# Performance work log

Measured on AMD Instinct MI355X. Metric: run time of the kernel, lower is better.

The kernel has to match this reference:

```python
import jax, jax.numpy as jnp
import numpy as np
from jax import lax

B, C, H, W = 256, 64, 48, 48   # batch, in_channels, spatial_dim, spatial_dim
E = 5                           # num_experts (ConditionalConv2D default)
DIM = 64 + 1                    # n_regulators + 1


def setup_inputs() -> dict:
    key = jax.random.key(0)
    ks = jax.random.split(key, 24)
    def n(k, shape, s=0.05):
        return jax.random.normal(k, shape, jnp.float32) * s
    inp = {
        "spatial_maps": jax.random.normal(ks[0], (B, C, H, W), jnp.float32),
        "cluster_info": jax.random.randint(ks[1], (B,), 0, C),
        # ConditionalConv2D (1x1, num_experts=5)
        "expert_w": n(ks[2], (E, C, C)),          # [experts, out_c, in_c] (1x1 squeezed)
        "cond_b": n(ks[3], (C,)),
        "route_emb": n(ks[4], (C, 4 * C)),        # Embedding(num_clusters=C, pool_emb=4C)
        "route_W": n(ks[5], (E, 8 * C)),          # Linear(2*pool_emb -> E)
        "route_b": n(ks[6], (E,)),
        # weight-normed conv stack (v, g, bias, prelu-a)
        "v1": n(ks[7], (32, C, 3, 3)),  "g1": jnp.ones((32,), jnp.float32),  "cb1": n(ks[8], (32,)),  "a1": jnp.array(0.1, jnp.float32),
        "v2": n(ks[9], (64, 32, 3, 3)), "g2": jnp.ones((64,), jnp.float32),  "cb2": n(ks[10], (64,)), "a2": jnp.array(0.1, jnp.float32),
        "v3": n(ks[11], (128, 64, 3, 3)), "g3": jnp.ones((128,), jnp.float32), "cb3": n(ks[12], (128,)), "a3": jnp.array(0.1, jnp.float32),
        # cluster embedding + alpha + MLP
        "emb2": n(ks[13], (C, 128)),
        "alpha": jnp.array(1.0, jnp.float32),
        "mW1": n(ks[14], (64, 128)), "mb1": n(ks[15], (64,)), "a4": jnp.array(0.1, jnp.float32),
        "mW2": n(ks[16], (32, 64)),  "mb2": n(ks[17], (32,)), "a5": jnp.array(0.1, jnp.float32),
        "mW3": n(ks[18], (DIM, 32)), "mb3": n(ks[19], (DIM,)),
    }
    return inp


def _wn(v, g):
    # weight_norm over all dims except 0 (torch default dim=0)
    nrm = jnp.sqrt((v * v).sum((1, 2, 3)))
    return v * (g / nrm)[:, None, None, None]


def _conv(x, w, b):
    y = lax.conv_general_dilated(x, w, (1, 1), 'SAME',
                                 dimension_numbers=('NCHW', 'OIHW', 'NCHW'))
    return y + b[None, :, None, None]


def _prelu(x, a):
    return jnp.where(x >= 0, x, a * x)


def _mpool(x):
    return lax.reduce_window(x, -jnp.inf, lax.max, (1, 1, 2, 2), (1, 1, 2, 2), 'VALID')


def reference(spatial_maps, cluster_info, expert_w, cond_b, route_emb, route_W, route_b,
              v1, g1, cb1, a1, v2, g2, cb2, a2, v3, g3, cb3, a3,
              emb2, alpha, mW1, mb1, a4, mW2, mb2, a5, mW3, mb3):
    x = spatial_maps
    # routing: adaptive avg pool (2,2), flatten, concat cluster embedding, linear, sigmoid
    pooled = x.reshape(B, C, 2, H // 2, 2, W // 2).mean((3, 5)).reshape(B, 4 * C)
    feat = jnp.concatenate([pooled, route_emb[cluster_info]], axis=1)      # [B, 8C]
    rw = jax.nn.sigmoid(feat @ route_W.T + route_b)                        # [B, E]
    # per-sample expert-mixed 1x1 kernel, applied as batched 1x1 conv
    kern = jnp.einsum('be,eoi->boi', rw, expert_w)                         # [B, C, C]
    cc = jnp.einsum('boi,bihw->bohw', kern, x) + cond_b[None, :, None, None]
    out = jax.nn.sigmoid(cc) * x                                           # attention gate
    # dense conv stack
    h = _mpool(_prelu(_conv(out, _wn(v1, g1), cb1), a1))
    h = _mpool(_prelu(_conv(h, _wn(v2, g2), cb2), a2))
    h = _mpool(_prelu(_conv(h, _wn(v3, g3), cb3), a3))
    h = h.mean((2, 3))                                                      # AdaptiveAvgPool2d(1)+Flatten -> [B,128]
    h = h + emb2[cluster_info] * alpha
    # MLP head
    h = _prelu(h @ mW1.T + mb1, a4)
    h = _prelu(h @ mW2.T + mb2, a5)
    return h @ mW3.T + mb3                                                  # [B, DIM]
```

## Files before the change

### kernel.cpp

```cpp
#include <hip/hip_runtime.h>


typedef _Float16 f16;
typedef f16 f16x8 __attribute__((ext_vector_type(8)));
typedef f16 f16x4 __attribute__((ext_vector_type(4)));
typedef f16 f16x2 __attribute__((ext_vector_type(2)));
typedef __fp16 h16x2 __attribute__((ext_vector_type(2)));
typedef float f32x4 __attribute__((ext_vector_type(4)));

constexpr size_t OFF_POOLED = 0;
constexpr size_t OFF_KERN   = 65536;
constexpr size_t OFF_W1     = 65536 + 1048576;
constexpr size_t OFF_W2     = OFF_W1 + 32*64*12;
constexpr size_t OFF_W3     = OFF_W2 + 64*32*12;
constexpr size_t OFF_H1     = OFF_W3 + 128*64*12;

__device__ __forceinline__ float sigmoidf_(float z) {
    return __builtin_amdgcn_rcpf(1.0f + __expf(-z));
}

__device__ __forceinline__ f16x2 pkrtz(float a, float b) {
    h16x2 r = __builtin_amdgcn_cvt_pkrtz(a, b);
    f16x2 o; o[0] = (f16)r[0]; o[1] = (f16)r[1];
    return o;
}

__device__ __forceinline__ void store_slot8(f16* glds, int row, int sc, int icg, const float* c) {
    f16x2 p0 = pkrtz(c[0], c[1]);
    f16x2 p1 = pkrtz(c[2], c[3]);
    f16x2 p2 = pkrtz(c[4], c[5]);
    f16x2 p3 = pkrtz(c[6], c[7]);
    f16x8 hv = { p0[0], p0[1], p1[0], p1[1], p2[0], p2[1], p3[0], p3[1] };
    *(f16x8*)&glds[(row * 50 + sc) * 64 + ((icg ^ (sc & 7)) << 3)] = hv;
}

__global__ void __launch_bounds__(64)
k_prep(const float* __restrict__ x,
       const float* __restrict__ v1, const float* __restrict__ g1,
       const float* __restrict__ v2, const float* __restrict__ g2,
       const float* __restrict__ v3, const float* __restrict__ g3,
       float* __restrict__ ws)
{
    const int blk = blockIdx.x;
    const int lane = threadIdx.x;
    if (blk < 16384) {
        const float4* p = (const float4*)(x + (size_t)blk * 2304);
        float a0 = 0.f, a1 = 0.f, a2 = 0.f, a3 = 0.f;
        #pragma unroll
        for (int j = 0; j < 9; j++) {
            int i = lane + 64 * j;
            int row = i / 12, cg = i - 12 * row;
            float4 v = p[i];
            float s = v.x + v.y + v.z + v.w;
            bool hq = (row >= 24), wq = (cg >= 6);
            a0 += (!hq && !wq) ? s : 0.f;
            a1 += (!hq &&  wq) ? s : 0.f;
            a2 += ( hq && !wq) ? s : 0.f;
            a3 += ( hq &&  wq) ? s : 0.f;
        }
        #pragma unroll
        for (int off = 32; off; off >>= 1) {
            a0 += __shfl_down(a0, off);
            a1 += __shfl_down(a1, off);
            a2 += __shfl_down(a2, off);
            a3 += __shfl_down(a3, off);
        }
        if (lane == 0) {
            int b = blk >> 6, c = blk & 63;
            float* d = ws + OFF_POOLED + (size_t)b * 256 + c * 4;
            d[0] = a0 * (1.0f / 576.0f);
            d[1] = a1 * (1.0f / 576.0f);
            d[2] = a2 * (1.0f / 576.0f);
            d[3] = a3 * (1.0f / 576.0f);
        }
    } else {
        int bo = blk - 16384;
        const float* v; const float* g; int IC, oc; int which;
        if (bo < 32)       { v = v1; g = g1; oc = bo;      IC = 64; which = 1; }
        else if (bo < 96)  { v = v2; g = g2; oc = bo - 32; IC = 32; which = 2; }
        else               { v = v3; g = g3; oc = bo - 96; IC = 64; which = 3; }
        int n = IC * 9;
        const float* vo = v + (size_t)oc * n;
        float s = 0.0f;
        for (int i = lane; i < n; i += 64) { float xv = vo[i]; s += xv * xv; }
        #pragma unroll
        for (int off = 32; off; off >>= 1) s += __shfl_down(s, off);
        float tot = __shfl(s, 0);
        float sc = g[oc] / sqrtf(tot);
        if (which == 1) {
            f16* o1 = (f16*)(ws + OFF_W1);
            for (int i = lane; i < n; i += 64) {
                int ic = i / 9, kk = i - ic * 9;
                o1[kk * 2048 + oc * 64 + (ic ^ ((oc & 7) << 3))] = (f16)(vo[i] * sc);
            }
        } else if (which == 2) {
            f16* o2 = (f16*)(ws + OFF_W2);
            for (int i = lane; i < n; i += 64) {
                int ic = i / 9, kk = i - ic * 9;
                o2[(kk * 64 + oc) * 32 + ic] = (f16)(vo[i] * sc);
            }
        } else {
            f16* o3 = (f16*)(ws + OFF_W3);
            for (int i = lane; i < n; i += 64) {
                int ic = i / 9, kk = i - ic * 9;
                o3[(kk * 128 + oc) * 64 + ic] = (f16)(vo[i] * sc);
            }
        }
    }
}

__global__ void k_route(const int* __restrict__ cluster,
                        const float* __restrict__ route_emb,
                        const float* __restrict__ route_W,
                        const float* __restrict__ route_b,
                        const float* __restrict__ expert_w,
                        float* __restrict__ ws)
{
    int b = blockIdx.x, t = threadIdx.x;
    __shared__ float feat[512];
    __shared__ float rwv[5];
    __shared__ float red[256];
    int cl = cluster[b];
    feat[t]       = ws[OFF_POOLED + (size_t)b * 256 + t];
    feat[256 + t] = route_emb[(size_t)cl * 256 + t];
    __syncthreads();
    float f0 = feat[t], f1 = feat[256 + t];
    for (int e = 0; e < 5; e++) {
        float pv = f0 * route_W[e * 512 + t] + f1 * route_W[e * 512 + 256 + t];
        red[t] = pv;
        __syncthreads();
        if (t < 128) red[t] += red[t + 128];
        __syncthreads();
        if (t < 64) {
            float s = red[t] + red[t + 64];
            #pragma unroll
            for (int off = 32; off; off >>= 1) s += __shfl_down(s, off);
            if (t == 0) rwv[e] = 1.0f / (1.0f + __expf(-(s + route_b[e])));
        }
        __syncthreads();
    }
    float r0 = rwv[0], r1 = rwv[1], r2 = rwv[2], r3 = rwv[3], r4 = rwv[4];
    f16* khg = (f16*)(ws + OFF_KERN);
    for (int j = t; j < 4096; j += 256) {
        int oc = j >> 6, ic = j & 63;
        float kv = r0 * expert_w[j] + r1 * expert_w[4096 + j] +
                   r2 * expert_w[2 * 4096 + j] + r3 * expert_w[3 * 4096 + j] +
                   r4 * expert_w[4 * 4096 + j];
        khg[(size_t)b * 4096 + oc * 64 + (ic ^ ((oc & 7) << 3))] = (f16)kv;
    }
}

__global__ void __launch_bounds__(512, 4)
k_f1(const float* __restrict__ x, const f16* __restrict__ kernH,
     const float* __restrict__ cond_b, const f16* __restrict__ w1H,
     const float* __restrict__ cb1, const float* __restrict__ a1,
     f16* __restrict__ h1h)
{
    extern __shared__ char smem[];
    f16*  glds  = (f16*)smem;
    f16*  kh    = (f16*)(smem + 64000);
    float* cbl  = (float*)(smem + 72192);
    f16*  hm    = (f16*)smem;
    f16*  poolt = (f16*)(smem + 16384);

    const int t = threadIdx.x;
    const int tile = blockIdx.x;
    const int b = blockIdx.y;
    const int r0 = tile * 8;
    const int w = t >> 6, l = t & 63;
    const int l15 = l & 15, agrp = l >> 4;

    ((uint4*)kh)[t] = ((const uint4*)(kernH + (size_t)b * 4096))[t];
    if (t < 64) cbl[t] = cond_b[t];
    if (t < 160) {
        int row = t >> 4, rem = t & 15;
        int col = (rem >= 8) ? 49 : 0;
        int slot = rem & 7;
        uint4 z = {};
        *(uint4*)&glds[(row * 50 + col) * 64 + slot * 8] = z;
    }
    for (int e = t; e < 960; e += 512) {
        int row = e / 96;
        int rem = e - row * 96;
        int colg = rem >> 3;
        int icg = rem & 7;
        int r_in = r0 - 1 + row;
        float4 va[8];
        if (r_in >= 0 && r_in < 48) {
            const float4* xp = (const float4*)x + ((size_t)(b * 64 + icg * 8)) * 576 + r_in * 12 + colg;
            #pragma unroll
            for (int i = 0; i < 8; i++) va[i] = xp[i * 576];
        } else {
            #pragma unroll
            for (int i = 0; i < 8; i++) va[i] = (float4){0.f, 0.f, 0.f, 0.f};
        }
        float c0[8], c1[8], c2c[8], c3[8];
        #pragma unroll
        for (int i = 0; i < 8; i++) { c0[i] = va[i].x; c1[i] = va[i].y; c2c[i] = va[i].z; c3[i] = va[i].w; }
        int scb = colg * 4 + 1;
        store_slot8(glds, row, scb + 0, icg, c0);
        store_slot8(glds, row, scb + 1, icg, c1);
        store_slot8(glds, row, scb + 2, icg, c2c);
        store_slot8(glds, row, scb + 3, icg, c3);
    }
    __syncthreads();

    {
        const int nt0 = (w < 6) ? 4 * w : 24 + 3 * (w - 6);
        const int NT  = (w < 6) ? 4 : 3;
        f32x4 acc[4][4] = {};
        int srA[4], scA[4];
        #pragma unroll
        for (int j = 0; j < 4; j++) {
            int ntc = nt0 + ((j < NT) ? j : 0);
            int p = ntc * 16 + l15;
            srA[j] = p / 48; scA[j] = p - 48 * srA[j] + 1;
        }
        #pragma unroll
        for (int ks = 0; ks < 2; ks++) {
            f16x8 kfr[4];
            #pragma unroll
            for (int mt = 0; mt < 4; mt++) {
                int oc = mt * 16 + l15;
                kfr[mt] = *(const f16x8*)&kh[oc * 64 + (((ks * 4 + agrp) ^ (oc & 7)) << 3)];
            }
            #pragma unroll
            for (int j = 0; j < 4; j++) {
                f16x8 bfr = *(const f16x8*)&glds[(srA[j] * 50 + scA[j]) * 64 +
                                                 (((ks * 4 + agrp) ^ (scA[j] & 7)) << 3)];
                #pragma unroll
                for (int mt = 0; mt < 4; mt++)
                    acc[mt][j] = __builtin_amdgcn_mfma_f32_16x16x32_f16(kfr[mt], bfr, acc[mt][j], 0, 0, 0);
            }
        }
        f32x4 cbv[4];
        #pragma unroll
        for (int mt = 0; mt < 4; mt++) cbv[mt] = *(const f32x4*)&cbl[mt * 16 + 4 * agrp];
        #pragma unroll
        for (int j = 0; j < 4; j++) {
            if (j < NT) {
                int base = (srA[j] * 50 + scA[j]) * 64;
                int sw8 = (scA[j] & 7) << 3;
                #pragma unroll
                for (int mt = 0; mt < 4; mt++) {
                    int oc0 = mt * 16 + 4 * agrp;
                    int addr = base + (oc0 ^ sw8);
                    f16x4 xv4 = *(const f16x4*)&glds[addr];
                    float s0 = sigmoidf_(acc[mt][j][0] + cbv[mt][0]);
                    float s1 = sigmoidf_(acc[mt][j][1] + cbv[mt][1]);
                    float s2 = sigmoidf_(acc[mt][j][2] + cbv[mt][2]);
                    float s3 = sigmoidf_(acc[mt][j][3] + cbv[mt][3]);
                    f16x2 slo = pkrtz(s0, s1);
                    f16x2 shi = pkrtz(s2, s3);
                    f16x2 xlo = { xv4[0], xv4[1] };
                    f16x2 xhi = { xv4[2], xv4[3] };
                    f16x2 glo = slo * xlo;
                    f16x2 ghi = shi * xhi;
                    f16x4 g4 = { glo[0], glo[1], ghi[0], ghi[1] };
                    *(f16x4*)&glds[addr] = g4;
                }
            }
        }
    }
    __syncthreads();

    f32x4 c2[3][2] = {};
    {
        const int q = w;
        #pragma unroll
        for (int kt = 0; kt < 18; kt++) {
            const int kk = kt >> 1, hh = kt & 1;
            const int dy = kk / 3, dx = kk - dy * 3;
            f16x8 bfr2[2];
            #pragma unroll
            for (int nt = 0; nt < 2; nt++) {
                int oc = nt * 16 + l15;
                int slot = (hh * 4 + agrp) ^ (oc & 7);
                bfr2[nt] = *(const f16x8*)&w1H[(kk * 32 + oc) * 64 + slot * 8];
            }
            #pragma unroll
            for (int mtl = 0; mtl < 3; mtl++) {
                int sc = mtl * 16 + l15 + dx;
                int slot = (hh * 4 + agrp) ^ (sc & 7);
                f16x8 af = *(const f16x8*)&glds[((q + dy) * 50 + sc) * 64 + slot * 8];
                c2[mtl][0] = __builtin_amdgcn_mfma_f32_16x16x32_f16(af, bfr2[0], c2[mtl][0], 0, 0, 0);
                c2[mtl][1] = __builtin_amdgcn_mfma_f32_16x16x32_f16(af, bfr2[1], c2[mtl][1], 0, 0, 0);
            }
        }
    }
    __syncthreads();

    {
        const int q = w;
        #pragma unroll
        for (int mtl = 0; mtl < 3; mtl++)
            #pragma unroll
            for (int nt = 0; nt < 2; nt++) {
                float h0 = fmaxf(c2[mtl][nt][0], c2[mtl][nt][1]);
                float h1 = fmaxf(c2[mtl][nt][2], c2[mtl][nt][3]);
                f16x2 hp = pkrtz(h0, h1);
                int oc = nt * 16 + l15;
                int pp = mtl * 8 + 2 * agrp;
                *(f16x2*)&hm[(q * 32 + oc) * 26 + pp] = hp;
            }
    }
    __syncthreads();

    {
        const float av = a1[0];
        #pragma unroll
        for (int k = 0; k < 6; k++) {
            int e = t + 512 * k;
            int oc = e & 31, pos2 = e >> 5;
            int pr = pos2 / 24, pc = pos2 - 24 * pr;
            float v0 = (float)hm[((2 * pr) * 32 + oc) * 26 + pc];
            float v1 = (float)hm[((2 * pr + 1) * 32 + oc) * 26 + pc];
            float v = fmaxf(v0, v1) + cb1[oc];
            v = (v >= 0.0f) ? v : av * v;
            poolt[pos2 * 40 + oc] = (f16)v;
        }
    }
    __syncthreads();

    if (t < 384) {
        int pos2 = t >> 2, slot = t & 3;
        uint4 val = *(const uint4*)&poolt[pos2 * 40 + slot * 8];
        ((uint4*)h1h)[((size_t)b * 576 + tile * 96 + pos2) * 4 + slot] = val;
    }
}

__global__ void __launch_bounds__(1024, 1)
k_f23(const f16* __restrict__ h1h, const f16* __restrict__ w2h,
      const float* __restrict__ cb2, const float* __restrict__ a2,
      const f16* __restrict__ w3h, const float* __restrict__ cb3, const float* __restrict__ a3,
      const int* __restrict__ cluster, const float* __restrict__ emb2, const float* __restrict__ alpha,
      const float* __restrict__ mW1, const float* __restrict__ mb1, const float* __restrict__ a4,
      const float* __restrict__ mW2, const float* __restrict__ mb2, const float* __restrict__ a5,
      const float* __restrict__ mW3, const float* __restrict__ mb3,
      float* __restrict__ out)
{
    extern __shared__ char smem[];
    f16*  x2    = (f16*)smem;
    f16*  h2l   = (f16*)(smem + 82944);
    float* ps   = (float*)(smem + 111168);
    float* hb   = (float*)(smem + 113216);
    float* t1   = (float*)(smem + 113728);
    float* t2   = (float*)(smem + 113984);
    f16*  dump2 = (f16*)smem;
    f16*  dump3 = (f16*)smem;

    const int b = blockIdx.x, t = threadIdx.x;
    const int w = t >> 6, l = t & 63;
    const int l15 = l & 15, agrp = l >> 4;

    for (int e = t; e < 400; e += 1024) {
        int bp = e >> 2, slot = e & 3;
        int r, c;
        if (bp < 26)      { r = 0;  c = bp; }
        else if (bp < 52) { r = 25; c = bp - 26; }
        else if (bp < 76) { r = bp - 52 + 1; c = 0; }
        else              { r = bp - 76 + 1; c = 25; }
        uint4 z = {};
        *(uint4*)&x2[(r * 26 + c) * 40 + slot * 8] = z;
    }
    for (int e = t; e < 416; e += 1024) {
        int bp = e >> 3, slot = e & 7;
        int r, c;
        if (bp < 14)      { r = 0;  c = bp; }
        else if (bp < 28) { r = 13; c = bp - 14; }
        else if (bp < 40) { r = bp - 28 + 1; c = 0; }
        else              { r = bp - 40 + 1; c = 13; }
        uint4 z = {};
        *(uint4*)&h2l[(r * 14 + c) * 72 + slot * 8] = z;
    }
    {
        const uint4* src = (const uint4*)(h1h + (size_t)b * 18432);
        for (int e = t; e < 2304; e += 1024) {
            int pos = e >> 2, slot = e & 3;
            int r = pos / 24, c = pos - 24 * r;
            *(uint4*)&x2[((r + 1) * 26 + (c + 1)) * 40 + slot * 8] = src[e];
        }
    }
    __syncthreads();

    const int m = w & 3, ng = w >> 2;
    f32x4 acc[9];
    {
        f16x8 afr[9];
        #pragma unroll
        for (int kk = 0; kk < 9; kk++)
            afr[kk] = *(const f16x8*)&w2h[(kk * 64 + m * 16 + l15) * 32 + agrp * 8];
        #pragma unroll
        for (int i = 0; i < 9; i++) acc[i] = (f32x4){0.f, 0.f, 0.f, 0.f};
        constexpr int K2[9] = {0, 40, 80, 26 * 40, 27 * 40, 28 * 40, 52 * 40, 53 * 40, 54 * 40};
        #pragma unroll
        for (int i = 0; i < 9; i++) {
            int p = (ng * 9 + i) * 16 + l15;
            int r = p / 24, c = p - 24 * r;
            int base = (r * 26 + c) * 40 + agrp * 8;
            #pragma unroll
            for (int kk = 0; kk < 9; kk++) {
                f16x8 bfr = *(const f16x8*)&x2[base + K2[kk]];
                acc[i] = __builtin_amdgcn_mfma_f32_16x16x32_f16(afr[kk], bfr, acc[i], 0, 0, 0);
            }
        }
    }
    __syncthreads();

    #pragma unroll
    for (int i = 0; i < 9; i++) {
        int p = (ng * 9 + i) * 16 + l15;
        f16x2 d0 = pkrtz(acc[i][0], acc[i][1]);
        f16x2 d1 = pkrtz(acc[i][2], acc[i][3]);
        f16x4 hv = { d0[0], d0[1], d1[0], d1[1] };
        *(f16x4*)&dump2[p * 72 + m * 16 + 4 * agrp] = hv;
    }
    __syncthreads();

    {
        const float a2v = a2[0];
        for (int e = t; e < 9216; e += 1024) {
            int oc = e & 63, pos2 = e >> 6;
            int pr = pos2 / 12, pc = pos2 - 12 * pr;
            int p0 = (2 * pr) * 24 + 2 * pc;
            float mm = fmaxf(fmaxf((float)dump2[p0 * 72 + oc], (float)dump2[(p0 + 1) * 72 + oc]),
                             fmaxf((float)dump2[(p0 + 24) * 72 + oc], (float)dump2[(p0 + 25) * 72 + oc]));
            float v = mm + cb2[oc];
            v = (v >= 0.0f) ? v : a2v * v;
            h2l[((pr + 1) * 14 + (pc + 1)) * 72 + oc] = (f16)v;
        }
    }
    __syncthreads();

    const int m8 = w & 7, ng3 = w >> 3;
    const int nt0c3 = ng3 * 5;
    const int cnt3  = ng3 ? 4 : 5;
    f32x4 acc3[5];
    {
        int pb[5];
        #pragma unroll
        for (int i = 0; i < 5; i++) {
            int p = (nt0c3 + i) * 16 + l15;
            int r = p / 12, c = p - 12 * r;
            pb[i] = ((r + 1) * 14 + (c + 1)) * 72 + agrp * 8;
            acc3[i] = (f32x4){0.f, 0.f, 0.f, 0.f};
        }
        constexpr int K3[9] = {-15 * 72, -14 * 72, -13 * 72, -72, 0, 72, 13 * 72, 14 * 72, 15 * 72};
        #pragma unroll
        for (int kk = 0; kk < 9; kk++) {
            #pragma unroll
            for (int ks = 0; ks < 2; ks++) {
                f16x8 afr = *(const f16x8*)&w3h[(size_t)(kk * 128 + m8 * 16 + l15) * 64 + ks * 32 + agrp * 8];
                #pragma unroll
                for (int i = 0; i < 5; i++) {
                    if (i < cnt3) {
                        f16x8 bfr = *(const f16x8*)&h2l[pb[i] + ks * 32 + K3[kk]];
                        acc3[i] = __builtin_amdgcn_mfma_f32_16x16x32_f16(afr, bfr, acc3[i], 0, 0, 0);
                    }
                }
            }
        }
    }
    #pragma unroll
    for (int i = 0; i < 5; i++) {
        if (i < cnt3) {
            int p = (nt0c3 + i) * 16 + l15;
            f16x2 d0 = pkrtz(acc3[i][0], acc3[i][1]);
            f16x2 d1 = pkrtz(acc3[i][2], acc3[i][3]);
            f16x4 hv = { d0[0], d0[1], d1[0], d1[1] };
            *(f16x4*)&dump3[p * 136 + m8 * 16 + 4 * agrp] = hv;
        }
    }
    __syncthreads();

    if (t < 512) {
        int oc = t >> 2, q = t & 3;
        int qr = q >> 1, qc = q & 1;
        const float a3v = a3[0];
        float cbv = cb3[oc];
        float s = 0.f;
        #pragma unroll
        for (int i = 0; i < 3; i++)
            #pragma unroll
            for (int j = 0; j < 3; j++) {
                int pr = 3 * qr + i, pc = 3 * qc + j;
                int p0 = (2 * pr) * 12 + 2 * pc;
                float mm = fmaxf(fmaxf((float)dump3[p0 * 136 + oc], (float)dump3[(p0 + 1) * 136 + oc]),
                                 fmaxf((float)dump3[(p0 + 12) * 136 + oc], (float)dump3[(p0 + 13) * 136 + oc]));
                float v = mm + cbv;
                v = (v >= 0.0f) ? v : a3v * v;
                s += v;
            }
        ps[t] = s;
    }
    __syncthreads();
    if (t < 128) {
        int cl = cluster[b];
        hb[t] = (ps[4 * t] + ps[4 * t + 1] + ps[4 * t + 2] + ps[4 * t + 3]) * (1.0f / 36.0f)
              + emb2[(size_t)cl * 128 + t] * alpha[0];
    }
    __syncthreads();
    if (t < 64) {
        const float4* wr = (const float4*)(mW1 + t * 128);
        float s = mb1[t];
        #pragma unroll 8
        for (int j = 0; j < 32; j++) {
            float4 wv4 = wr[j];
            s += wv4.x * hb[4 * j] + wv4.y * hb[4 * j + 1] + wv4.z * hb[4 * j + 2] + wv4.w * hb[4 * j + 3];
        }
        float a4v = a4[0];
        t1[t] = (s >= 0.0f) ? s : a4v * s;
    }
    __syncthreads();
    if (t < 32) {
        const float4* wr = (const float4*)(mW2 + t * 64);
        float s = mb2[t];
        #pragma unroll
        for (int j = 0; j < 16; j++) {
            float4 wv4 = wr[j];
            s += wv4.x * t1[4 * j] + wv4.y * t1[4 * j + 1] + wv4.z * t1[4 * j + 2] + wv4.w * t1[4 * j + 3];
        }
        float a5v = a5[0];
        t2[t] = (s >= 0.0f) ? s : a5v * s;
    }
    __syncthreads();
    if (t < 65) {
        const float4* wr = (const float4*)(mW3 + t * 32);
        float s = mb3[t];
        #pragma unroll
        for (int j = 0; j < 8; j++) {
            float4 wv4 = wr[j];
            s += wv4.x * t2[4 * j] + wv4.y * t2[4 * j + 1] + wv4.z * t2[4 * j + 2] + wv4.w * t2[4 * j + 3];
        }
        out[(size_t)b * 65 + t] = s;
    }
}

extern "C" void kernel_launch(void* const* d_in, const int* in_sizes, int n_in,
                              void* d_out, int out_size, void* d_ws, size_t ws_size,
                              hipStream_t stream)
{
    const float* x         = (const float*)d_in[0];
    const int*   cluster   = (const int*)  d_in[1];
    const float* expert_w  = (const float*)d_in[2];
    const float* cond_b    = (const float*)d_in[3];
    const float* route_emb = (const float*)d_in[4];
    const float* route_W   = (const float*)d_in[5];
    const float* route_b   = (const float*)d_in[6];
    const float* v1  = (const float*)d_in[7];
    const float* g1  = (const float*)d_in[8];
    const float* cb1 = (const float*)d_in[9];
    const float* a1  = (const float*)d_in[10];
    const float* v2  = (const float*)d_in[11];
    const float* g2  = (const float*)d_in[12];
    const float* cb2 = (const float*)d_in[13];
    const float* a2  = (const float*)d_in[14];
    const float* v3  = (const float*)d_in[15];
    const float* g3  = (const float*)d_in[16];
    const float* cb3 = (const float*)d_in[17];
    const float* a3  = (const float*)d_in[18];
    const float* emb2  = (const float*)d_in[19];
    const float* alpha = (const float*)d_in[20];
    const float* mW1 = (const float*)d_in[21];
    const float* mb1 = (const float*)d_in[22];
    const float* a4  = (const float*)d_in[23];
    const float* mW2 = (const float*)d_in[24];
    const float* mb2 = (const float*)d_in[25];
    const float* a5  = (const float*)d_in[26];
    const float* mW3 = (const float*)d_in[27];
    const float* mb3 = (const float*)d_in[28];
    float* ws  = (float*)d_ws;
    float* out = (float*)d_out;

    hipFuncSetAttribute((const void*)k_f1,  hipFuncAttributeMaxDynamicSharedMemorySize, 72448);
    hipFuncSetAttribute((const void*)k_f23, hipFuncAttributeMaxDynamicSharedMemorySize, 114112);

    k_prep<<<16608, 64, 0, stream>>>(x, v1, g1, v2, g2, v3, g3, ws);
    k_route<<<256, 256, 0, stream>>>(cluster, route_emb, route_W, route_b, expert_w, ws);
    k_f1<<<dim3(6, 256), 512, 72448, stream>>>(x, (const f16*)(ws + OFF_KERN), cond_b,
                                               (const f16*)(ws + OFF_W1), cb1, a1,
                                               (f16*)(ws + OFF_H1));
    k_f23<<<256, 1024, 114112, stream>>>((const f16*)(ws + OFF_H1), (const f16*)(ws + OFF_W2),
                                         cb2, a2, (const f16*)(ws + OFF_W3), cb3, a3,
                                         cluster, emb2, alpha,
                                         mW1, mb1, a4, mW2, mb2, a5, mW3, mb3, out);
}
```

Baseline: 119.0 us.

## Halve conv1 row tile to four rows and redistribute wave work for occupancy

The fused gate+conv1 kernel now processes 4 output rows per block instead of 8, doubling the grid and shrinking LDS from about 72KB to about 47KB. Launch bounds rise to 6 blocks per CU. The MFMA work is redistributed unevenly across waves to match the smaller tile, and the input-loading loop index order is changed. The per-sample expert kernel is copied into LDS with a direct global-to-LDS load. This raises occupancy and latency hiding, at the cost of more halo rows reloaded per output row and lower per-wave MFMA utilisation, since some waves do less work.

```diff
diff --git a/kernel.cpp b/kernel.cpp
--- a/kernel.cpp
+++ b/kernel.cpp
@@ -150,7 +150,7 @@
     }
 }
 
-__global__ void __launch_bounds__(512, 4)
+__global__ void __launch_bounds__(512, 6)
 k_f1(const float* __restrict__ x, const f16* __restrict__ kernH,
      const float* __restrict__ cond_b, const f16* __restrict__ w1H,
      const float* __restrict__ cb1, const float* __restrict__ a1,
@@ -158,32 +158,36 @@
 {
     extern __shared__ char smem[];
     f16*  glds  = (f16*)smem;
-    f16*  kh    = (f16*)(smem + 64000);
-    float* cbl  = (float*)(smem + 72192);
+    f16*  kh    = (f16*)(smem + 38400);
+    float* cbl  = (float*)(smem + 46592);
     f16*  hm    = (f16*)smem;
-    f16*  poolt = (f16*)(smem + 16384);
+    f16*  poolt = (f16*)(smem + 8192);
 
     const int t = threadIdx.x;
     const int tile = blockIdx.x;
     const int b = blockIdx.y;
-    const int r0 = tile * 8;
+    const int r0 = tile * 4;
     const int w = t >> 6, l = t & 63;
     const int l15 = l & 15, agrp = l >> 4;
 
-    ((uint4*)kh)[t] = ((const uint4*)(kernH + (size_t)b * 4096))[t];
+    {
+        const f16* src = kernH + (size_t)b * 4096 + w * 512 + l * 8;
+        __builtin_amdgcn_global_load_lds((const uint32_t*)src,
+                                         (uint32_t*)(kh + w * 512), 16, 0, 0);
+    }
     if (t < 64) cbl[t] = cond_b[t];
-    if (t < 160) {
+    if (t < 96) {
         int row = t >> 4, rem = t & 15;
         int col = (rem >= 8) ? 49 : 0;
         int slot = rem & 7;
         uint4 z = {};
         *(uint4*)&glds[(row * 50 + col) * 64 + slot * 8] = z;
     }
-    for (int e = t; e < 960; e += 512) {
+    for (int e = t; e < 576; e += 512) {
         int row = e / 96;
         int rem = e - row * 96;
-        int colg = rem >> 3;
-        int icg = rem & 7;
+        int icg = rem / 12;
+        int colg = rem - icg * 12;
         int r_in = r0 - 1 + row;
         float4 va[8];
         if (r_in >= 0 && r_in < 48) {
@@ -206,12 +210,12 @@
     __syncthreads();
 
     {
-        const int nt0 = (w < 6) ? 4 * w : 24 + 3 * (w - 6);
-        const int NT  = (w < 6) ? 4 : 3;
-        f32x4 acc[4][4] = {};
-        int srA[4], scA[4];
-        #pragma unroll
-        for (int j = 0; j < 4; j++) {
+        const int nt0 = (w < 2) ? 3 * w : 6 + 2 * (w - 2);
+        const int NT  = (w < 2) ? 3 : 2;
+        f32x4 acc[4][3] = {};
+        int srA[3], scA[3];
+        #pragma unroll
+        for (int j = 0; j < 3; j++) {
             int ntc = nt0 + ((j < NT) ? j : 0);
             int p = ntc * 16 + l15;
             srA[j] = p / 48; scA[j] = p - 48 * srA[j] + 1;
@@ -225,7 +229,7 @@
                 kfr[mt] = *(const f16x8*)&kh[oc * 64 + (((ks * 4 + agrp) ^ (oc & 7)) << 3)];
             }
             #pragma unroll
-            for (int j = 0; j < 4; j++) {
+            for (int j = 0; j < 3; j++) {
                 f16x8 bfr = *(const f16x8*)&glds[(srA[j] * 50 + scA[j]) * 64 +
                                                  (((ks * 4 + agrp) ^ (scA[j] & 7)) << 3)];
                 #pragma unroll
@@ -237,7 +241,7 @@
         #pragma unroll
         for (int mt = 0; mt < 4; mt++) cbv[mt] = *(const f32x4*)&cbl[mt * 16 + 4 * agrp];
         #pragma unroll
-        for (int j = 0; j < 4; j++) {
+        for (int j = 0; j < 3; j++) {
             if (j < NT) {
                 int base = (srA[j] * 50 + scA[j]) * 64;
                 int sw8 = (scA[j] & 7) << 3;
@@ -264,9 +268,15 @@
     }
     __syncthreads();
 
-    f32x4 c2[3][2] = {};
-    {
-        const int q = w;
+    const int U = (w < 4) ? 2 : 1;
+    f32x4 c2[2][2] = {};
+    int qU[2], mtlU[2];
+    #pragma unroll
+    for (int i = 0; i < 2; i++) {
+        int u = (w < 4) ? (2 * w + ((i < U) ? i : 0)) : (8 + (w - 4));
+        qU[i] = u / 3; mtlU[i] = u - 3 * qU[i];
+    }
+    {
         #pragma unroll
         for (int kt = 0; kt < 18; kt++) {
             const int kk = kt >> 1, hh = kt & 1;
@@ -279,37 +289,39 @@
                 bfr2[nt] = *(const f16x8*)&w1H[(kk * 32 + oc) * 64 + slot * 8];
             }
             #pragma unroll
-            for (int mtl = 0; mtl < 3; mtl++) {
-                int sc = mtl * 16 + l15 + dx;
-                int slot = (hh * 4 + agrp) ^ (sc & 7);
-                f16x8 af = *(const f16x8*)&glds[((q + dy) * 50 + sc) * 64 + slot * 8];
-                c2[mtl][0] = __builtin_amdgcn_mfma_f32_16x16x32_f16(af, bfr2[0], c2[mtl][0], 0, 0, 0);
-                c2[mtl][1] = __builtin_amdgcn_mfma_f32_16x16x32_f16(af, bfr2[1], c2[mtl][1], 0, 0, 0);
-            }
-        }
-    }
-    __syncthreads();
-
-    {
-        const int q = w;
-        #pragma unroll
-        for (int mtl = 0; mtl < 3; mtl++)
+            for (int i = 0; i < 2; i++) {
+                if (i < U) {
+                    int sc = mtlU[i] * 16 + l15 + dx;
+                    int slot = (hh * 4 + agrp) ^ (sc & 7);
+                    f16x8 af = *(const f16x8*)&glds[((qU[i] + dy) * 50 + sc) * 64 + slot * 8];
+                    c2[i][0] = __builtin_amdgcn_mfma_f32_16x16x32_f16(af, bfr2[0], c2[i][0], 0, 0, 0);
+                    c2[i][1] = __builtin_amdgcn_mfma_f32_16x16x32_f16(af, bfr2[1], c2[i][1], 0, 0, 0);
+                }
+            }
+        }
+    }
+    __syncthreads();
+
+    #pragma unroll
+    for (int i = 0; i < 2; i++) {
+        if (i < U) {
             #pragma unroll
             for (int nt = 0; nt < 2; nt++) {
-                float h0 = fmaxf(c2[mtl][nt][0], c2[mtl][nt][1]);
-                float h1 = fmaxf(c2[mtl][nt][2], c2[mtl][nt][3]);
+                float h0 = fmaxf(c2[i][nt][0], c2[i][nt][1]);
+                float h1 = fmaxf(c2[i][nt][2], c2[i][nt][3]);
                 f16x2 hp = pkrtz(h0, h1);
                 int oc = nt * 16 + l15;
-                int pp = mtl * 8 + 2 * agrp;
-                *(f16x2*)&hm[(q * 32 + oc) * 26 + pp] = hp;
-            }
+                int pp = mtlU[i] * 8 + 2 * agrp;
+                *(f16x2*)&hm[(qU[i] * 32 + oc) * 26 + pp] = hp;
+            }
+        }
     }
     __syncthreads();
 
     {
         const float av = a1[0];
         #pragma unroll
-        for (int k = 0; k < 6; k++) {
+        for (int k = 0; k < 3; k++) {
             int e = t + 512 * k;
             int oc = e & 31, pos2 = e >> 5;
             int pr = pos2 / 24, pc = pos2 - 24 * pr;
@@ -322,10 +334,10 @@
     }
     __syncthreads();
 
-    if (t < 384) {
+    if (t < 192) {
         int pos2 = t >> 2, slot = t & 3;
         uint4 val = *(const uint4*)&poolt[pos2 * 40 + slot * 8];
-        ((uint4*)h1h)[((size_t)b * 576 + tile * 96 + pos2) * 4 + slot] = val;
+        ((uint4*)h1h)[((size_t)b * 576 + tile * 48 + pos2) * 4 + slot] = val;
     }
 }
 
@@ -572,14 +584,14 @@
     float* ws  = (float*)d_ws;
     float* out = (float*)d_out;
 
-    hipFuncSetAttribute((const void*)k_f1,  hipFuncAttributeMaxDynamicSharedMemorySize, 72448);
+    hipFuncSetAttribute((const void*)k_f1,  hipFuncAttributeMaxDynamicSharedMemorySize, 46848);
     hipFuncSetAttribute((const void*)k_f23, hipFuncAttributeMaxDynamicSharedMemorySize, 114112);
 
     k_prep<<<16608, 64, 0, stream>>>(x, v1, g1, v2, g2, v3, g3, ws);
     k_route<<<256, 256, 0, stream>>>(cluster, route_emb, route_W, route_b, expert_w, ws);
-    k_f1<<<dim3(6, 256), 512, 72448, stream>>>(x, (const f16*)(ws + OFF_KERN), cond_b,
-                                               (const f16*)(ws + OFF_W1), cb1, a1,
-                                               (f16*)(ws + OFF_H1));
+    k_f1<<<dim3(12, 256), 512, 46848, stream>>>(x, (const f16*)(ws + OFF_KERN), cond_b,
+                                                (const f16*)(ws + OFF_W1), cb1, a1,
+                                                (f16*)(ws + OFF_H1));
     k_f23<<<256, 1024, 114112, stream>>>((const f16*)(ws + OFF_H1), (const f16*)(ws + OFF_W2),
                                          cb2, a2, (const f16*)(ws + OFF_W3), cb3, a3,
                                          cluster, emb2, alpha,
```

Result: slower. 172.3 us (+44.7%).
